# Kernel tuning notes

Measured on AMD Instinct MI355X. Metric: run time of the kernel, lower is better.

## Reference

```python
import jax, jax.numpy as jnp
import numpy as np

LEVELS = np.array([8, 5, 5, 5], dtype=np.int64)
BASIS = np.cumprod(np.concatenate([[1], LEVELS[:-1]])).astype(np.int64)  # [1,8,40,200]
N_E = int(np.prod(LEVELS))  # 1000
BN_EPS = 1e-5
BOUND_EPS = 1e-3


def setup_inputs() -> dict:
    key = jax.random.key(0)
    ks = jax.random.split(key, 3)
    B, C, T, E = 32, 512, 4096, 4
    return {
        "z": jax.random.normal(ks[0], (B, C, T), dtype=jnp.float32),
        "W_in": jax.random.normal(ks[1], (C, E), dtype=jnp.float32) * 0.05,
        "b_in": jnp.zeros((E,), dtype=jnp.float32),
        "gamma": jnp.ones((E,), dtype=jnp.float32),
        "beta": jnp.zeros((E,), dtype=jnp.float32),
        "W_out": jax.random.normal(ks[2], (E, C), dtype=jnp.float32) * 0.05,
        "b_out": jnp.zeros((C,), dtype=jnp.float32),
    }


def _round_ste(x):
    return x + jax.lax.stop_gradient(jnp.round(x) - x)


def reference(z, W_in, b_in, gamma, beta, W_out, b_out):
    levels = jnp.asarray(LEVELS, dtype=jnp.float32)      # [E]
    basis = jnp.asarray(BASIS, dtype=jnp.float32)        # [E]
    half_w = jnp.floor(levels / 2.0)                     # levels // 2
    B, C, T = z.shape
    N = B * T

    # preprocess: 'n c t -> (n t) c'
    x = jnp.transpose(z, (0, 2, 1)).reshape(N, C)        # [N, C]
    # project_in
    h = x @ W_in + b_in                                   # [N, E]
    # BatchNorm1d, training mode (biased batch stats)
    mu = jnp.mean(h, axis=0)
    var = jnp.var(h, axis=0)
    h = (h - mu) * jax.lax.rsqrt(var + BN_EPS) * gamma + beta

    # bound + round_ste quantize
    half_l = (levels - 1.0) * (1.0 - BOUND_EPS) / 2.0
    offset = jnp.where(jnp.mod(levels, 2.0) == 0.0, 0.5, 0.0)
    shift = jnp.tan(offset / half_l)
    bounded = jnp.tanh(h + shift) * half_l - offset
    zhat_n = _round_ste(bounded) / half_w                 # [N, E], normalized codes

    # codes -> indices
    idx = jnp.sum((zhat_n * half_w + half_w) * basis, axis=-1).astype(jnp.int32)  # [N]

    # project_out, '(b t) c -> b c t'
    out = zhat_n @ W_out + b_out                          # [N, C]
    zhat = jnp.transpose(out.reshape(B, T, C), (0, 2, 1))  # [B, C, T]

    commit_loss = jnp.mean((z - jax.lax.stop_gradient(zhat)) ** 2)

    # perplexity via counts (avoids [N, n_e] one-hot)
    counts = jnp.zeros((N_E,), dtype=jnp.float32).at[idx].add(1.0)
    e_mean = counts / N
    perplexity = jnp.exp(-jnp.sum(e_mean * jnp.log(e_mean + 1e-10)))

    return zhat, commit_loss, perplexity
```

## Files before the change

### kernel.cpp

```cpp
#include <hip/hip_runtime.h>
#include <math.h>


namespace {
constexpr int Bv = 32, Cv = 512, Tv = 4096;
constexpr int Nv = Bv * Tv;
constexpr long long TOTv = (long long)Nv * Cv;
constexpr int NTILES = Nv / 256;
constexpr int CSPLIT = 4;
constexpr int CL = Cv / CSPLIT;

constexpr size_t OFF_H   = 0;
constexpr size_t OFF_G   = OFF_H  + (size_t)Nv * 4 * sizeof(double);
constexpr size_t OFF_BS  = OFF_G  + (size_t)Nv * 4 * sizeof(float);
constexpr size_t OFF_CST = OFF_BS + (size_t)NTILES * 10 * sizeof(double);
constexpr size_t OFF_CNT = OFF_CST + 32 * sizeof(double);
constexpr size_t OFF_CP  = OFF_CNT + 4096;
constexpr size_t OFF_WD  = OFF_CP  + (size_t)NTILES * sizeof(double);
constexpr size_t OFF_WT  = OFF_WD  + 2048 * sizeof(double);
}

__global__ void fsq_k0(const float* __restrict__ W_in, const float* __restrict__ W_out,
                       double* __restrict__ winD, float* __restrict__ woutT)
{
    const int i = blockIdx.x * 256 + threadIdx.x;
    if (i < 2048) {
        winD[i] = (double)W_in[i];
        const int c = i >> 2, e = i & 3;
        woutT[i] = W_out[e * 512 + c];
    }
}

__global__ __launch_bounds__(256) void fsq_kA(
    const float* __restrict__ z, const double* __restrict__ winD,
    const float* __restrict__ woutT, const float* __restrict__ b_out,
    const float* __restrict__ b_in,
    double* __restrict__ h_ws, float* __restrict__ g_ws, double* __restrict__ bs_ws)
{
    __shared__ double red[256][10];
    const int tid = threadIdx.x;
    const int blk = blockIdx.x;
    const int b = blk >> 4;
    const int tile = blk & 15;
    const int t = tile * 256 + tid;
    const float* zp = z + (size_t)b * Cv * Tv + t;

    double h0 = 0.0, h1 = 0.0, h2 = 0.0, h3 = 0.0;
    float g0 = 0.f, g1 = 0.f, g2 = 0.f, g3 = 0.f, zbp = 0.f, z2p = 0.f;
#pragma unroll 8
    for (int c = 0; c < Cv; ++c) {
        const float zv = zp[(size_t)c * Tv];
        const double zd = (double)zv;
        h0 = fma(zd, winD[c * 4 + 0], h0);
        h1 = fma(zd, winD[c * 4 + 1], h1);
        h2 = fma(zd, winD[c * 4 + 2], h2);
        h3 = fma(zd, winD[c * 4 + 3], h3);
        g0 = fmaf(zv, woutT[c * 4 + 0], g0);
        g1 = fmaf(zv, woutT[c * 4 + 1], g1);
        g2 = fmaf(zv, woutT[c * 4 + 2], g2);
        g3 = fmaf(zv, woutT[c * 4 + 3], g3);
        zbp = fmaf(zv, b_out[c], zbp);
        z2p = fmaf(zv, zv, z2p);
    }
    h0 += (double)b_in[0]; h1 += (double)b_in[1];
    h2 += (double)b_in[2]; h3 += (double)b_in[3];

    const int n = blk * 256 + tid;
    double* hp = h_ws + (size_t)n * 4;
    double2 hA; hA.x = h0; hA.y = h1;
    double2 hB; hB.x = h2; hB.y = h3;
    *(double2*)(hp)     = hA;
    *(double2*)(hp + 2) = hB;
    *(float4*)(g_ws + (size_t)n * 4) = make_float4(g0, g1, g2, g3);

    red[tid][0] = h0; red[tid][1] = h1; red[tid][2] = h2; red[tid][3] = h3;
    red[tid][4] = h0 * h0; red[tid][5] = h1 * h1; red[tid][6] = h2 * h2; red[tid][7] = h3 * h3;
    red[tid][8] = (double)z2p; red[tid][9] = (double)zbp;
    __syncthreads();
    for (int s = 128; s > 0; s >>= 1) {
        if (tid < s) {
#pragma unroll
            for (int k = 0; k < 10; ++k) red[tid][k] += red[tid + s][k];
        }
        __syncthreads();
    }
    if (tid == 0) {
#pragma unroll
        for (int k = 0; k < 10; ++k) bs_ws[blk * 10 + k] = red[0][k];
    }
}

__global__ __launch_bounds__(512) void fsq_kB(
    const float* __restrict__ gamma, const float* __restrict__ beta,
    const float* __restrict__ W_out, const float* __restrict__ b_out,
    const double* __restrict__ bs_ws, double* __restrict__ consts,
    unsigned* __restrict__ counts)
{
    __shared__ double buf[512 * 15];
    const int tid = threadIdx.x;
#pragma unroll
    for (int k = 0; k < 10; ++k) buf[tid * 15 + k] = bs_ws[tid * 10 + k];
    __syncthreads();
    for (int s = 256; s > 0; s >>= 1) {
        if (tid < s) {
#pragma unroll
            for (int k = 0; k < 10; ++k) buf[tid * 15 + k] += buf[(tid + s) * 15 + k];
        }
        __syncthreads();
    }
    double Sh[4] = {0, 0, 0, 0}, Sq[4] = {0, 0, 0, 0}, SZ2 = 0, SZB = 0;
    if (tid == 0) {
        Sh[0] = buf[0]; Sh[1] = buf[1]; Sh[2] = buf[2]; Sh[3] = buf[3];
        Sq[0] = buf[4]; Sq[1] = buf[5]; Sq[2] = buf[6]; Sq[3] = buf[7];
        SZ2 = buf[8]; SZB = buf[9];
    }
    __syncthreads();
    {
        const int c = tid;
        const double w0 = W_out[c], w1 = W_out[512 + c], w2 = W_out[1024 + c], w3 = W_out[1536 + c];
        const double bb = b_out[c];
        double* r = buf + tid * 15;
        r[0] = w0 * w0; r[1] = w0 * w1; r[2] = w0 * w2; r[3] = w0 * w3;
        r[4] = w1 * w1; r[5] = w1 * w2; r[6] = w1 * w3;
        r[7] = w2 * w2; r[8] = w2 * w3; r[9] = w3 * w3;
        r[10] = w0 * bb; r[11] = w1 * bb; r[12] = w2 * bb; r[13] = w3 * bb; r[14] = bb * bb;
    }
    __syncthreads();
    for (int s = 256; s > 0; s >>= 1) {
        if (tid < s) {
#pragma unroll
            for (int k = 0; k < 15; ++k) buf[tid * 15 + k] += buf[(tid + s) * 15 + k];
        }
        __syncthreads();
    }
    if (tid == 0) {
        const double Ninv = 1.0 / (double)Nv;
#pragma unroll
        for (int e = 0; e < 4; ++e) {
            const double mu = Sh[e] * Ninv;
            const double var = Sq[e] * Ninv - mu * mu;
            const double sc = (double)gamma[e] / sqrt(var + 1e-5);
            consts[e] = sc;
            consts[4 + e] = (double)beta[e] - mu * sc;
        }
        consts[8 + 0]  = buf[0]; consts[8 + 1]  = buf[1]; consts[8 + 2]  = buf[2]; consts[8 + 3]  = buf[3];
        consts[8 + 4]  = buf[1]; consts[8 + 5]  = buf[4]; consts[8 + 6]  = buf[5]; consts[8 + 7]  = buf[6];
        consts[8 + 8]  = buf[2]; consts[8 + 9]  = buf[5]; consts[8 + 10] = buf[7]; consts[8 + 11] = buf[8];
        consts[8 + 12] = buf[3]; consts[8 + 13] = buf[6]; consts[8 + 14] = buf[8]; consts[8 + 15] = buf[9];
        consts[24] = buf[10]; consts[25] = buf[11]; consts[26] = buf[12]; consts[27] = buf[13];
        consts[28] = buf[14];
        consts[29] = SZ2; consts[30] = SZB;
        consts[31] = tan(0.5 / ((8.0 - 1.0) * (1.0 - 1e-3) / 2.0));
    }
    for (int i = tid; i < 1000; i += 512) counts[i] = 0;
}

__global__ __launch_bounds__(256) void fsq_kC(
    const float* __restrict__ woutT, const float* __restrict__ b_out,
    const double* __restrict__ h_ws, const float* __restrict__ g_ws,
    const double* __restrict__ consts, unsigned* __restrict__ counts,
    double* __restrict__ cp_ws, float* __restrict__ out)
{
    __shared__ double red[256];
    const int tid = threadIdx.x;
    const int nt = blockIdx.x;
    const int ys = blockIdx.y;
    const int n = nt * 256 + tid;

    const double sc0 = consts[0], sc1 = consts[1], sc2 = consts[2], sc3 = consts[3];
    const double bi0 = consts[4], bi1 = consts[5], bi2 = consts[6], bi3 = consts[7];
    const double shift0 = consts[31];

    const double* hp = h_ws + (size_t)n * 4;
    const double hn0 = fma(hp[0], sc0, bi0);
    const double hn1 = fma(hp[1], sc1, bi1);
    const double hn2 = fma(hp[2], sc2, bi2);
    const double hn3 = fma(hp[3], sc3, bi3);

    constexpr double hl0 = (8.0 - 1.0) * (1.0 - 1e-3) / 2.0;
    constexpr double hl1 = (5.0 - 1.0) * (1.0 - 1e-3) / 2.0;
    const double r0 = rint(tanh(hn0 + shift0) * hl0 - 0.5);
    const double r1 = rint(tanh(hn1) * hl1);
    const double r2 = rint(tanh(hn2) * hl1);
    const double r3 = rint(tanh(hn3) * hl1);
    const double zd0 = r0 * 0.25, zd1 = r1 * 0.5, zd2 = r2 * 0.5, zd3 = r3 * 0.5;
    const float zn0 = (float)zd0, zn1 = (float)zd1, zn2 = (float)zd2, zn3 = (float)zd3;

    if (ys == 0) {
        const int code = ((int)r0 + 4) + ((int)r1 + 2) * 8 + ((int)r2 + 2) * 40 + ((int)r3 + 2) * 200;
        atomicAdd(&counts[code], 1u);
        const float4 gv = *(const float4*)(g_ws + (size_t)n * 4);
        const double cg = zd0 * (double)gv.x + zd1 * (double)gv.y
                        + zd2 * (double)gv.z + zd3 * (double)gv.w;
        const double znd[4] = {zd0, zd1, zd2, zd3};
        double q = consts[28] + 2.0 * (zd0 * consts[24] + zd1 * consts[25]
                                     + zd2 * consts[26] + zd3 * consts[27]);
#pragma unroll
        for (int e = 0; e < 4; ++e)
#pragma unroll
            for (int f = 0; f < 4; ++f)
                q = fma(znd[e] * znd[f], consts[8 + e * 4 + f], q);
        red[tid] = q - 2.0 * cg;
        __syncthreads();
        for (int s = 128; s > 0; s >>= 1) {
            if (tid < s) red[tid] += red[tid + s];
            __syncthreads();
        }
        if (tid == 0) cp_ws[nt] = red[0];
    }

    const int c0 = ys * CL;
    const size_t base = (size_t)(n >> 12) * ((size_t)Cv * Tv) + (size_t)(n & (Tv - 1));
#pragma unroll 8
    for (int i = 0; i < CL; ++i) {
        const int c = c0 + i;
        float val = b_out[c];
        val = fmaf(zn0, woutT[c * 4 + 0], val);
        val = fmaf(zn1, woutT[c * 4 + 1], val);
        val = fmaf(zn2, woutT[c * 4 + 2], val);
        val = fmaf(zn3, woutT[c * 4 + 3], val);
        out[base + (size_t)c * Tv] = val;
    }
}

__global__ __launch_bounds__(512) void fsq_kD(
    const double* __restrict__ cp_ws, const double* __restrict__ consts,
    const unsigned* __restrict__ counts, float* __restrict__ out, int out_size)
{
    __shared__ double rc[512];
    __shared__ double rp[512];
    const int tid = threadIdx.x;
    double c_ = cp_ws[tid];
    double p_ = 0.0;
    for (int i = tid; i < 1000; i += 512) {
        const double em = (double)counts[i] / (double)Nv;
        p_ += em * log(em + 1e-10);
    }
    rc[tid] = c_; rp[tid] = p_;
    __syncthreads();
    for (int s = 256; s > 0; s >>= 1) {
        if (tid < s) { rc[tid] += rc[tid + s]; rp[tid] += rp[tid + s]; }
        __syncthreads();
    }
    if (tid == 0) {
        const double commit = (consts[29] - 2.0 * consts[30] + rc[0]) / (double)TOTv;
        out[out_size - 2] = (float)commit;
        out[out_size - 1] = (float)exp(-rp[0]);
    }
}

extern "C" void kernel_launch(void* const* d_in, const int* in_sizes, int n_in,
                              void* d_out, int out_size, void* d_ws, size_t ws_size,
                              hipStream_t stream) {
    const float* z     = (const float*)d_in[0];
    const float* W_in  = (const float*)d_in[1];
    const float* b_in  = (const float*)d_in[2];
    const float* gamma = (const float*)d_in[3];
    const float* beta  = (const float*)d_in[4];
    const float* W_out = (const float*)d_in[5];
    const float* b_out = (const float*)d_in[6];
    float* out = (float*)d_out;

    char* ws = (char*)d_ws;
    double*   h_ws   = (double*)(ws + OFF_H);
    float*    g_ws   = (float*)(ws + OFF_G);
    double*   bs_ws  = (double*)(ws + OFF_BS);
    double*   consts = (double*)(ws + OFF_CST);
    unsigned* counts = (unsigned*)(ws + OFF_CNT);
    double*   cp_ws  = (double*)(ws + OFF_CP);
    double*   winD   = (double*)(ws + OFF_WD);
    float*    woutT  = (float*)(ws + OFF_WT);

    fsq_k0<<<8, 256, 0, stream>>>(W_in, W_out, winD, woutT);
    fsq_kA<<<NTILES, 256, 0, stream>>>(z, winD, woutT, b_out, b_in, h_ws, g_ws, bs_ws);
    fsq_kB<<<1, 512, 0, stream>>>(gamma, beta, W_out, b_out, bs_ws, consts, counts);
    fsq_kC<<<dim3(NTILES, CSPLIT), 256, 0, stream>>>(woutT, b_out, h_ws, g_ws, consts,
                                                     counts, cp_ws, out);
    fsq_kD<<<1, 512, 0, stream>>>(cp_ws, consts, counts, out, out_size);
}
```

Baseline: 177.0 us.

## Fuse all stages into one cooperative persistent kernel with grid syncs

Replaces the five kernel launches with a single cooperative kernel of 512 blocks × 128 threads. Each thread handles two time steps and keeps its projections in registers across grid.sync(), so the h/g workspace round trip through global memory goes away. Weights are staged in shared memory, and the projection is now computed in fp32 instead of fp64. Block reductions become wavefront shuffles. The cost is reliance on cooperative launch: the whole grid must be co-resident, with fewer threads per block, and the lower precision may shift rounding at quantization boundaries.

After: 298.6 us. 1.69x slower.

```diff
diff --git a/kernel.cpp b/kernel.cpp
--- a/kernel.cpp
+++ b/kernel.cpp
@@ -1,251 +1,233 @@
 #include <hip/hip_runtime.h>
+#include <hip/hip_cooperative_groups.h>
 #include <math.h>
 
+namespace cg = cooperative_groups;
+
 
 namespace {
-constexpr int Bv = 32, Cv = 512, Tv = 4096;
+constexpr int Cv = 512, Tv = 4096, Bv = 32;
 constexpr int Nv = Bv * Tv;
 constexpr long long TOTv = (long long)Nv * Cv;
-constexpr int NTILES = Nv / 256;
-constexpr int CSPLIT = 4;
-constexpr int CL = Cv / CSPLIT;
-
-constexpr size_t OFF_H   = 0;
-constexpr size_t OFF_G   = OFF_H  + (size_t)Nv * 4 * sizeof(double);
-constexpr size_t OFF_BS  = OFF_G  + (size_t)Nv * 4 * sizeof(float);
-constexpr size_t OFF_CST = OFF_BS + (size_t)NTILES * 10 * sizeof(double);
-constexpr size_t OFF_CNT = OFF_CST + 32 * sizeof(double);
-constexpr size_t OFF_CP  = OFF_CNT + 4096;
-constexpr size_t OFF_WD  = OFF_CP  + (size_t)NTILES * sizeof(double);
-constexpr size_t OFF_WT  = OFF_WD  + 2048 * sizeof(double);
+constexpr int NBLK = 512;
+constexpr int NWAVE = NBLK * 2;
+
+constexpr size_t OFF_BS = 0;
+constexpr size_t OFF_GR = OFF_BS + (size_t)NWAVE * 10 * 8;
+constexpr size_t OFF_CP = OFF_GR + 16 * 8;
+constexpr size_t OFF_CT = OFF_CP + (size_t)NWAVE * 8;
 }
 
-__global__ void fsq_k0(const float* __restrict__ W_in, const float* __restrict__ W_out,
-                       double* __restrict__ winD, float* __restrict__ woutT)
+__global__ __launch_bounds__(128) void fsq_main(
+    const float* __restrict__ z, const float* __restrict__ W_in,
+    const float* __restrict__ b_in, const float* __restrict__ gamma,
+    const float* __restrict__ beta, const float* __restrict__ W_out,
+    const float* __restrict__ b_out, float* __restrict__ out,
+    double* __restrict__ bs, double* __restrict__ gram,
+    double* __restrict__ cp, unsigned* __restrict__ counts, int out_size)
 {
-    const int i = blockIdx.x * 256 + threadIdx.x;
-    if (i < 2048) {
-        winD[i] = (double)W_in[i];
-        const int c = i >> 2, e = i & 3;
-        woutT[i] = W_out[e * 512 + c];
-    }
-}
-
-__global__ __launch_bounds__(256) void fsq_kA(
-    const float* __restrict__ z, const double* __restrict__ winD,
-    const float* __restrict__ woutT, const float* __restrict__ b_out,
-    const float* __restrict__ b_in,
-    double* __restrict__ h_ws, float* __restrict__ g_ws, double* __restrict__ bs_ws)
-{
-    __shared__ double red[256][10];
+    cg::grid_group grid = cg::this_grid();
+    __shared__ float s_wi[512][4];
+    __shared__ float s_wo[512][4];
+    __shared__ float s_bo[512];
+
     const int tid = threadIdx.x;
-    const int blk = blockIdx.x;
-    const int b = blk >> 4;
-    const int tile = blk & 15;
-    const int t = tile * 256 + tid;
-    const float* zp = z + (size_t)b * Cv * Tv + t;
-
-    double h0 = 0.0, h1 = 0.0, h2 = 0.0, h3 = 0.0;
-    float g0 = 0.f, g1 = 0.f, g2 = 0.f, g3 = 0.f, zbp = 0.f, z2p = 0.f;
+    const int lane = tid & 63;
+    const int bid = blockIdx.x;
+    const int wid = bid * 2 + (tid >> 6);
+    const int b = bid >> 4;
+    const int t0 = (bid & 15) << 8;
+
+    if (bid == 0) {
+        for (int i = tid; i < 1000; i += 128) counts[i] = 0;
+    }
+    for (int i = tid; i < 512; i += 128) {
+        *(float4*)&s_wi[i][0] = *(const float4*)(W_in + i * 4);
+        s_wo[i][0] = W_out[i];
+        s_wo[i][1] = W_out[512 + i];
+        s_wo[i][2] = W_out[1024 + i];
+        s_wo[i][3] = W_out[1536 + i];
+        s_bo[i] = b_out[i];
+    }
+    __syncthreads();
+
+    float h[2][4] = {}, g[2][4] = {};
+    float z2 = 0.f, zbp = 0.f;
+    const float* zp = z + (size_t)b * Cv * Tv + t0 + tid * 2;
 #pragma unroll 8
-    for (int c = 0; c < Cv; ++c) {
-        const float zv = zp[(size_t)c * Tv];
-        const double zd = (double)zv;
-        h0 = fma(zd, winD[c * 4 + 0], h0);
-        h1 = fma(zd, winD[c * 4 + 1], h1);
-        h2 = fma(zd, winD[c * 4 + 2], h2);
-        h3 = fma(zd, winD[c * 4 + 3], h3);
-        g0 = fmaf(zv, woutT[c * 4 + 0], g0);
-        g1 = fmaf(zv, woutT[c * 4 + 1], g1);
-        g2 = fmaf(zv, woutT[c * 4 + 2], g2);
-        g3 = fmaf(zv, woutT[c * 4 + 3], g3);
-        zbp = fmaf(zv, b_out[c], zbp);
-        z2p = fmaf(zv, zv, z2p);
-    }
-    h0 += (double)b_in[0]; h1 += (double)b_in[1];
-    h2 += (double)b_in[2]; h3 += (double)b_in[3];
-
-    const int n = blk * 256 + tid;
-    double* hp = h_ws + (size_t)n * 4;
-    double2 hA; hA.x = h0; hA.y = h1;
-    double2 hB; hB.x = h2; hB.y = h3;
-    *(double2*)(hp)     = hA;
-    *(double2*)(hp + 2) = hB;
-    *(float4*)(g_ws + (size_t)n * 4) = make_float4(g0, g1, g2, g3);
-
-    red[tid][0] = h0; red[tid][1] = h1; red[tid][2] = h2; red[tid][3] = h3;
-    red[tid][4] = h0 * h0; red[tid][5] = h1 * h1; red[tid][6] = h2 * h2; red[tid][7] = h3 * h3;
-    red[tid][8] = (double)z2p; red[tid][9] = (double)zbp;
-    __syncthreads();
-    for (int s = 128; s > 0; s >>= 1) {
-        if (tid < s) {
-#pragma unroll
-            for (int k = 0; k < 10; ++k) red[tid][k] += red[tid + s][k];
-        }
-        __syncthreads();
-    }
-    if (tid == 0) {
-#pragma unroll
-        for (int k = 0; k < 10; ++k) bs_ws[blk * 10 + k] = red[0][k];
-    }
-}
-
-__global__ __launch_bounds__(512) void fsq_kB(
-    const float* __restrict__ gamma, const float* __restrict__ beta,
-    const float* __restrict__ W_out, const float* __restrict__ b_out,
-    const double* __restrict__ bs_ws, double* __restrict__ consts,
-    unsigned* __restrict__ counts)
-{
-    __shared__ double buf[512 * 15];
-    const int tid = threadIdx.x;
-#pragma unroll
-    for (int k = 0; k < 10; ++k) buf[tid * 15 + k] = bs_ws[tid * 10 + k];
-    __syncthreads();
-    for (int s = 256; s > 0; s >>= 1) {
-        if (tid < s) {
-#pragma unroll
-            for (int k = 0; k < 10; ++k) buf[tid * 15 + k] += buf[(tid + s) * 15 + k];
-        }
-        __syncthreads();
-    }
-    double Sh[4] = {0, 0, 0, 0}, Sq[4] = {0, 0, 0, 0}, SZ2 = 0, SZB = 0;
-    if (tid == 0) {
-        Sh[0] = buf[0]; Sh[1] = buf[1]; Sh[2] = buf[2]; Sh[3] = buf[3];
-        Sq[0] = buf[4]; Sq[1] = buf[5]; Sq[2] = buf[6]; Sq[3] = buf[7];
-        SZ2 = buf[8]; SZB = buf[9];
-    }
-    __syncthreads();
+    for (int c = 0; c < 512; ++c) {
+        const float2 zv = *(const float2*)(zp + (size_t)c * Tv);
+        const float4 wi = *(const float4*)&s_wi[c][0];
+        const float4 wo = *(const float4*)&s_wo[c][0];
+        const float bo = s_bo[c];
+        const float zr[2] = {zv.x, zv.y};
+#pragma unroll
+        for (int j = 0; j < 2; ++j) {
+            h[j][0] = fmaf(zr[j], wi.x, h[j][0]);
+            h[j][1] = fmaf(zr[j], wi.y, h[j][1]);
+            h[j][2] = fmaf(zr[j], wi.z, h[j][2]);
+            h[j][3] = fmaf(zr[j], wi.w, h[j][3]);
+            g[j][0] = fmaf(zr[j], wo.x, g[j][0]);
+            g[j][1] = fmaf(zr[j], wo.y, g[j][1]);
+            g[j][2] = fmaf(zr[j], wo.z, g[j][2]);
+            g[j][3] = fmaf(zr[j], wo.w, g[j][3]);
+            z2 = fmaf(zr[j], zr[j], z2);
+        }
+        zbp = fmaf(zv.x + zv.y, bo, zbp);
+    }
     {
-        const int c = tid;
-        const double w0 = W_out[c], w1 = W_out[512 + c], w2 = W_out[1024 + c], w3 = W_out[1536 + c];
-        const double bb = b_out[c];
-        double* r = buf + tid * 15;
-        r[0] = w0 * w0; r[1] = w0 * w1; r[2] = w0 * w2; r[3] = w0 * w3;
-        r[4] = w1 * w1; r[5] = w1 * w2; r[6] = w1 * w3;
-        r[7] = w2 * w2; r[8] = w2 * w3; r[9] = w3 * w3;
-        r[10] = w0 * bb; r[11] = w1 * bb; r[12] = w2 * bb; r[13] = w3 * bb; r[14] = bb * bb;
-    }
-    __syncthreads();
-    for (int s = 256; s > 0; s >>= 1) {
-        if (tid < s) {
-#pragma unroll
-            for (int k = 0; k < 15; ++k) buf[tid * 15 + k] += buf[(tid + s) * 15 + k];
-        }
-        __syncthreads();
-    }
-    if (tid == 0) {
+        const float bi0 = b_in[0], bi1 = b_in[1], bi2 = b_in[2], bi3 = b_in[3];
+#pragma unroll
+        for (int j = 0; j < 2; ++j) {
+            h[j][0] += bi0; h[j][1] += bi1; h[j][2] += bi2; h[j][3] += bi3;
+        }
+    }
+
+    {
+        double st[10];
+#pragma unroll
+        for (int e = 0; e < 4; ++e) {
+            const double h0 = (double)h[0][e], h1 = (double)h[1][e];
+            st[e] = h0 + h1;
+            st[4 + e] = h0 * h0 + h1 * h1;
+        }
+        st[8] = (double)z2; st[9] = (double)zbp;
+#pragma unroll
+        for (int k = 0; k < 10; ++k) {
+#pragma unroll
+            for (int m = 1; m < 64; m <<= 1) st[k] += __shfl_xor(st[k], m, 64);
+        }
+        if (lane == 0) {
+#pragma unroll
+            for (int k = 0; k < 10; ++k) bs[(size_t)wid * 10 + k] = st[k];
+        }
+    }
+
+    if (bid == NBLK - 1 && tid < 64) {
+        double a[15] = {};
+        for (int k = 0; k < 8; ++k) {
+            const int c = lane + k * 64;
+            const double w0 = (double)W_out[c], w1 = (double)W_out[512 + c];
+            const double w2 = (double)W_out[1024 + c], w3 = (double)W_out[1536 + c];
+            const double bb = (double)b_out[c];
+            a[0] += w0 * w0; a[1] += w0 * w1; a[2] += w0 * w2; a[3] += w0 * w3;
+            a[4] += w1 * w1; a[5] += w1 * w2; a[6] += w1 * w3;
+            a[7] += w2 * w2; a[8] += w2 * w3; a[9] += w3 * w3;
+            a[10] += w0 * bb; a[11] += w1 * bb; a[12] += w2 * bb; a[13] += w3 * bb;
+            a[14] += bb * bb;
+        }
+#pragma unroll
+        for (int k = 0; k < 15; ++k) {
+#pragma unroll
+            for (int m = 1; m < 64; m <<= 1) a[k] += __shfl_xor(a[k], m, 64);
+        }
+        if (lane == 0) {
+#pragma unroll
+            for (int k = 0; k < 15; ++k) gram[k] = a[k];
+        }
+    }
+
+    grid.sync();
+
+    double a8[8] = {};
+    for (int k = 0; k < 16; ++k) {
+        const double* r = bs + (size_t)(lane + k * 64) * 10;
+#pragma unroll
+        for (int q = 0; q < 8; ++q) a8[q] += r[q];
+    }
+#pragma unroll
+    for (int q = 0; q < 8; ++q) {
+#pragma unroll
+        for (int m = 1; m < 64; m <<= 1) a8[q] += __shfl_xor(a8[q], m, 64);
+    }
+    double sc[4], bi[4];
+    {
         const double Ninv = 1.0 / (double)Nv;
 #pragma unroll
         for (int e = 0; e < 4; ++e) {
-            const double mu = Sh[e] * Ninv;
-            const double var = Sq[e] * Ninv - mu * mu;
-            const double sc = (double)gamma[e] / sqrt(var + 1e-5);
-            consts[e] = sc;
-            consts[4 + e] = (double)beta[e] - mu * sc;
-        }
-        consts[8 + 0]  = buf[0]; consts[8 + 1]  = buf[1]; consts[8 + 2]  = buf[2]; consts[8 + 3]  = buf[3];
-        consts[8 + 4]  = buf[1]; consts[8 + 5]  = buf[4]; consts[8 + 6]  = buf[5]; consts[8 + 7]  = buf[6];
-        consts[8 + 8]  = buf[2]; consts[8 + 9]  = buf[5]; consts[8 + 10] = buf[7]; consts[8 + 11] = buf[8];
-        consts[8 + 12] = buf[3]; consts[8 + 13] = buf[6]; consts[8 + 14] = buf[8]; consts[8 + 15] = buf[9];
-        consts[24] = buf[10]; consts[25] = buf[11]; consts[26] = buf[12]; consts[27] = buf[13];
-        consts[28] = buf[14];
-        consts[29] = SZ2; consts[30] = SZB;
-        consts[31] = tan(0.5 / ((8.0 - 1.0) * (1.0 - 1e-3) / 2.0));
-    }
-    for (int i = tid; i < 1000; i += 512) counts[i] = 0;
-}
-
-__global__ __launch_bounds__(256) void fsq_kC(
-    const float* __restrict__ woutT, const float* __restrict__ b_out,
-    const double* __restrict__ h_ws, const float* __restrict__ g_ws,
-    const double* __restrict__ consts, unsigned* __restrict__ counts,
-    double* __restrict__ cp_ws, float* __restrict__ out)
-{
-    __shared__ double red[256];
-    const int tid = threadIdx.x;
-    const int nt = blockIdx.x;
-    const int ys = blockIdx.y;
-    const int n = nt * 256 + tid;
-
-    const double sc0 = consts[0], sc1 = consts[1], sc2 = consts[2], sc3 = consts[3];
-    const double bi0 = consts[4], bi1 = consts[5], bi2 = consts[6], bi3 = consts[7];
-    const double shift0 = consts[31];
-
-    const double* hp = h_ws + (size_t)n * 4;
-    const double hn0 = fma(hp[0], sc0, bi0);
-    const double hn1 = fma(hp[1], sc1, bi1);
-    const double hn2 = fma(hp[2], sc2, bi2);
-    const double hn3 = fma(hp[3], sc3, bi3);
+            const double mu = a8[e] * Ninv;
+            const double var = a8[4 + e] * Ninv - mu * mu;
+            sc[e] = (double)gamma[e] / sqrt(var + 1e-5);
+            bi[e] = (double)beta[e] - mu * sc[e];
+        }
+    }
+    double gr[15];
+#pragma unroll
+    for (int k = 0; k < 15; ++k) gr[k] = gram[k];
 
     constexpr double hl0 = (8.0 - 1.0) * (1.0 - 1e-3) / 2.0;
     constexpr double hl1 = (5.0 - 1.0) * (1.0 - 1e-3) / 2.0;
-    const double r0 = rint(tanh(hn0 + shift0) * hl0 - 0.5);
-    const double r1 = rint(tanh(hn1) * hl1);
-    const double r2 = rint(tanh(hn2) * hl1);
-    const double r3 = rint(tanh(hn3) * hl1);
-    const double zd0 = r0 * 0.25, zd1 = r1 * 0.5, zd2 = r2 * 0.5, zd3 = r3 * 0.5;
-    const float zn0 = (float)zd0, zn1 = (float)zd1, zn2 = (float)zd2, zn3 = (float)zd3;
-
-    if (ys == 0) {
-        const int code = ((int)r0 + 4) + ((int)r1 + 2) * 8 + ((int)r2 + 2) * 40 + ((int)r3 + 2) * 200;
+    const double shift0 = tan(0.5 / hl0);
+
+    float zn[2][4];
+    double qsum = 0.0;
+#pragma unroll
+    for (int j = 0; j < 2; ++j) {
+        const double hn0 = fma((double)h[j][0], sc[0], bi[0]);
+        const double hn1 = fma((double)h[j][1], sc[1], bi[1]);
+        const double hn2 = fma((double)h[j][2], sc[2], bi[2]);
+        const double hn3 = fma((double)h[j][3], sc[3], bi[3]);
+        const double r0 = rint(tanh(hn0 + shift0) * hl0 - 0.5);
+        const double r1 = rint(tanh(hn1) * hl1);
+        const double r2 = rint(tanh(hn2) * hl1);
+        const double r3 = rint(tanh(hn3) * hl1);
+        const double zd0 = r0 * 0.25, zd1 = r1 * 0.5, zd2 = r2 * 0.5, zd3 = r3 * 0.5;
+        zn[j][0] = (float)zd0; zn[j][1] = (float)zd1;
+        zn[j][2] = (float)zd2; zn[j][3] = (float)zd3;
+        const int code = ((int)r0 + 4) + ((int)r1 + 2) * 8 + ((int)r2 + 2) * 40
+                       + ((int)r3 + 2) * 200;
         atomicAdd(&counts[code], 1u);
-        const float4 gv = *(const float4*)(g_ws + (size_t)n * 4);
-        const double cg = zd0 * (double)gv.x + zd1 * (double)gv.y
-                        + zd2 * (double)gv.z + zd3 * (double)gv.w;
-        const double znd[4] = {zd0, zd1, zd2, zd3};
-        double q = consts[28] + 2.0 * (zd0 * consts[24] + zd1 * consts[25]
-                                     + zd2 * consts[26] + zd3 * consts[27]);
-#pragma unroll
-        for (int e = 0; e < 4; ++e)
-#pragma unroll
-            for (int f = 0; f < 4; ++f)
-                q = fma(znd[e] * znd[f], consts[8 + e * 4 + f], q);
-        red[tid] = q - 2.0 * cg;
-        __syncthreads();
-        for (int s = 128; s > 0; s >>= 1) {
-            if (tid < s) red[tid] += red[tid + s];
-            __syncthreads();
-        }
-        if (tid == 0) cp_ws[nt] = red[0];
-    }
-
-    const int c0 = ys * CL;
-    const size_t base = (size_t)(n >> 12) * ((size_t)Cv * Tv) + (size_t)(n & (Tv - 1));
-#pragma unroll 8
-    for (int i = 0; i < CL; ++i) {
-        const int c = c0 + i;
-        float val = b_out[c];
-        val = fmaf(zn0, woutT[c * 4 + 0], val);
-        val = fmaf(zn1, woutT[c * 4 + 1], val);
-        val = fmaf(zn2, woutT[c * 4 + 2], val);
-        val = fmaf(zn3, woutT[c * 4 + 3], val);
-        out[base + (size_t)c * Tv] = val;
-    }
-}
-
-__global__ __launch_bounds__(512) void fsq_kD(
-    const double* __restrict__ cp_ws, const double* __restrict__ consts,
-    const unsigned* __restrict__ counts, float* __restrict__ out, int out_size)
-{
-    __shared__ double rc[512];
-    __shared__ double rp[512];
-    const int tid = threadIdx.x;
-    double c_ = cp_ws[tid];
-    double p_ = 0.0;
-    for (int i = tid; i < 1000; i += 512) {
-        const double em = (double)counts[i] / (double)Nv;
-        p_ += em * log(em + 1e-10);
-    }
-    rc[tid] = c_; rp[tid] = p_;
-    __syncthreads();
-    for (int s = 256; s > 0; s >>= 1) {
-        if (tid < s) { rc[tid] += rc[tid + s]; rp[tid] += rp[tid + s]; }
-        __syncthreads();
-    }
-    if (tid == 0) {
-        const double commit = (consts[29] - 2.0 * consts[30] + rc[0]) / (double)TOTv;
-        out[out_size - 2] = (float)commit;
-        out[out_size - 1] = (float)exp(-rp[0]);
+        const double cg = zd0 * (double)g[j][0] + zd1 * (double)g[j][1]
+                        + zd2 * (double)g[j][2] + zd3 * (double)g[j][3];
+        double q = gr[14]
+                 + 2.0 * (zd0 * gr[10] + zd1 * gr[11] + zd2 * gr[12] + zd3 * gr[13])
+                 + zd0 * zd0 * gr[0] + zd1 * zd1 * gr[4]
+                 + zd2 * zd2 * gr[7] + zd3 * zd3 * gr[9]
+                 + 2.0 * (zd0 * zd1 * gr[1] + zd0 * zd2 * gr[2] + zd0 * zd3 * gr[3]
+                        + zd1 * zd2 * gr[5] + zd1 * zd3 * gr[6] + zd2 * zd3 * gr[8]);
+        qsum += q - 2.0 * cg;
+    }
+#pragma unroll
+    for (int m = 1; m < 64; m <<= 1) qsum += __shfl_xor(qsum, m, 64);
+    if (lane == 0) cp[wid] = qsum;
+
+    float* op = out + (size_t)b * Cv * Tv + t0 + tid * 2;
+#pragma unroll 4
+    for (int c = 0; c < 512; ++c) {
+        const float4 wo = *(const float4*)&s_wo[c][0];
+        const float bo = s_bo[c];
+        float2 o;
+        o.x = fmaf(zn[0][0], wo.x, fmaf(zn[0][1], wo.y,
+              fmaf(zn[0][2], wo.z, fmaf(zn[0][3], wo.w, bo))));
+        o.y = fmaf(zn[1][0], wo.x, fmaf(zn[1][1], wo.y,
+              fmaf(zn[1][2], wo.z, fmaf(zn[1][3], wo.w, bo))));
+        *(float2*)(op + (size_t)c * Tv) = o;
+    }
+
+    grid.sync();
+
+    if (bid == 0 && tid < 64) {
+        double csv = 0.0, z2t = 0.0, zbt = 0.0, pl = 0.0;
+        for (int k = 0; k < 16; ++k) {
+            csv += cp[lane + k * 64];
+            const double* r = bs + (size_t)(lane + k * 64) * 10;
+            z2t += r[8]; zbt += r[9];
+        }
+        for (int i = lane; i < 1000; i += 64) {
+            const double em = (double)counts[i] / (double)Nv;
+            pl += em * log(em + 1e-10);
+        }
+#pragma unroll
+        for (int m = 1; m < 64; m <<= 1) {
+            csv += __shfl_xor(csv, m, 64);
+            z2t += __shfl_xor(z2t, m, 64);
+            zbt += __shfl_xor(zbt, m, 64);
+            pl  += __shfl_xor(pl,  m, 64);
+        }
+        if (lane == 0) {
+            out[out_size - 2] = (float)((z2t - 2.0 * zbt + csv) / (double)TOTv);
+            out[out_size - 1] = (float)exp(-pl);
+        }
     }
 }
 
@@ -262,19 +244,13 @@
     float* out = (float*)d_out;
 
     char* ws = (char*)d_ws;
-    double*   h_ws   = (double*)(ws + OFF_H);
-    float*    g_ws   = (float*)(ws + OFF_G);
-    double*   bs_ws  = (double*)(ws + OFF_BS);
-    double*   consts = (double*)(ws + OFF_CST);
-    unsigned* counts = (unsigned*)(ws + OFF_CNT);
-    double*   cp_ws  = (double*)(ws + OFF_CP);
-    double*   winD   = (double*)(ws + OFF_WD);
-    float*    woutT  = (float*)(ws + OFF_WT);
-
-    fsq_k0<<<8, 256, 0, stream>>>(W_in, W_out, winD, woutT);
-    fsq_kA<<<NTILES, 256, 0, stream>>>(z, winD, woutT, b_out, b_in, h_ws, g_ws, bs_ws);
-    fsq_kB<<<1, 512, 0, stream>>>(gamma, beta, W_out, b_out, bs_ws, consts, counts);
-    fsq_kC<<<dim3(NTILES, CSPLIT), 256, 0, stream>>>(woutT, b_out, h_ws, g_ws, consts,
-                                                     counts, cp_ws, out);
-    fsq_kD<<<1, 512, 0, stream>>>(cp_ws, consts, counts, out, out_size);
+    double*   bs     = (double*)(ws + OFF_BS);
+    double*   gram   = (double*)(ws + OFF_GR);
+    double*   cp     = (double*)(ws + OFF_CP);
+    unsigned* counts = (unsigned*)(ws + OFF_CT);
+
+    void* args[] = {(void*)&z, (void*)&W_in, (void*)&b_in, (void*)&gamma, (void*)&beta,
+                    (void*)&W_out, (void*)&b_out, (void*)&out, (void*)&bs, (void*)&gram,
+                    (void*)&cp, (void*)&counts, (void*)&out_size};
+    hipLaunchCooperativeKernel((void*)fsq_main, dim3(NBLK), dim3(128), args, 0, stream);
 }
```
